# Optimization experiments

Measured on AMD Instinct MI355X. Metric: run time of the kernel, lower is better.

## Reference

```python
import jax, jax.numpy as jnp
import numpy as np

N_NODES = 100000
N_EDGES = 640000
D_IN = 128
D_OUT = 128


def setup_inputs() -> dict:
    key = jax.random.key(0)
    k1, k2, k3, k4, k5 = jax.random.split(key, 5)
    feats = jax.random.normal(k1, (N_NODES, D_IN), dtype=jnp.float32)
    src = jax.random.randint(k2, (N_EDGES,), 0, N_NODES, dtype=jnp.int32)
    dst = jax.random.randint(k3, (N_EDGES,), 0, N_NODES, dtype=jnp.int32)
    # Xavier-normal-ish init (gain for relu = sqrt(2))
    std = float(np.sqrt(2.0) * np.sqrt(2.0 / (D_IN + D_OUT)))
    linear_skip_weight = jax.random.normal(k4, (D_OUT, D_IN), dtype=jnp.float32) * std
    linear_msg_weight = jax.random.normal(k5, (D_OUT, D_IN), dtype=jnp.float32) * std
    linear_skip_bias = jnp.zeros((D_OUT,), dtype=jnp.float32)
    linear_msg_bias = jnp.zeros((D_OUT,), dtype=jnp.float32)
    return {
        "feats": feats,
        "src": src,
        "dst": dst,
        "linear_skip_weight": linear_skip_weight,
        "linear_skip_bias": linear_skip_bias,
        "linear_msg_weight": linear_msg_weight,
        "linear_msg_bias": linear_msg_bias,
    }


def reference(feats, src, dst, linear_skip_weight, linear_skip_bias,
              linear_msg_weight, linear_msg_bias):
    n = feats.shape[0]
    # degree from scatter-add of edge weights (ones) at source rows
    deg = jax.ops.segment_sum(jnp.ones_like(src, dtype=feats.dtype), src,
                              num_segments=n)
    deg_inv_sqrt = jnp.where(deg > 0, jax.lax.rsqrt(jnp.maximum(deg, 1.0)) * (deg > 0), 0.0)
    deg_inv_sqrt = jnp.where(deg > 0, deg ** -0.5, 0.0)
    # normalize source features, gather along edges, scatter-sum to dst
    feat_src = feats * deg_inv_sqrt[:, None]           # [N, D_IN]
    msgs = feat_src[src]                               # [E, D_IN]
    rst = jax.ops.segment_sum(msgs, dst, num_segments=n)  # [N, D_IN]
    rst = rst * deg_inv_sqrt[:, None]
    rst_ = rst @ linear_msg_weight.T + linear_msg_bias
    skip_x = feats @ linear_skip_weight.T + linear_skip_bias
    return rst_ + skip_x
```

## Files before the change

kernel.cpp:

```cpp
#include <hip/hip_runtime.h>

#define N_NODES 100000
#define N_EDGES 640000
#define D 128
#define NB ((N_NODES + 1023) / 1024)
#define BKT_C 16
#define OVF_CAP 32768

typedef short v8s __attribute__((ext_vector_type(8)));
typedef float v4f __attribute__((ext_vector_type(4)));

__device__ __forceinline__ unsigned short f2bf(float x) {
    unsigned int u = __builtin_bit_cast(unsigned int, x);
    u += 0x7fffu + ((u >> 16) & 1u);
    return (unsigned short)(u >> 16);
}
__device__ __forceinline__ float bf2f(unsigned int hi) {
    return __builtin_bit_cast(float, hi << 16);
}

__global__ __launch_bounds__(256) void k_zero(int4* __restrict__ pk4,
                                              int* __restrict__ ovf_cnt) {
    int i = blockIdx.x * blockDim.x + threadIdx.x;
    if (i < N_NODES / 4) pk4[i] = make_int4(0, 0, 0, 0);
    if (i == 0) *ovf_cnt = 0;
}

__global__ __launch_bounds__(256) void k_pre(const float* __restrict__ feats,
                                             const float* __restrict__ Wm,
                                             const float* __restrict__ Ws,
                                             const float* __restrict__ bmsg,
                                             const float* __restrict__ bskip,
                                             const int* __restrict__ src,
                                             const int* __restrict__ dst,
                                             unsigned int* __restrict__ pk,
                                             unsigned short* __restrict__ Bcat,
                                             float* __restrict__ bias,
                                             char* __restrict__ outb,
                                             int* __restrict__ bucket,
                                             int* __restrict__ ovf_cnt,
                                             int2* __restrict__ ovf) {
    int i = blockIdx.x * blockDim.x + threadIdx.x;
    if (i < D * D) {
        int j = i >> 7;
        int k = i & 127;
        Bcat[j * 256 + k]       = f2bf(Wm[i]);
        Bcat[j * 256 + 128 + k] = f2bf(Ws[i]);
    }
    if (i < D) bias[i] = bmsg[i] + bskip[i];
    if (i < N_EDGES) {
        int s = src[i];
        int d = dst[i];
        atomicAdd(&pk[s], 1u);
        unsigned int old = atomicAdd(&pk[d], 0x10000u);
        if (bucket) {
            unsigned int p = old >> 16;
            if (p < BKT_C) {
                bucket[d * BKT_C + (int)p] = s;
            } else {
                int q = atomicAdd(ovf_cnt, 1);
                if (q < OVF_CAP) ovf[q] = make_int2(d, s);
            }
        }
    }
    int g = i * 8;
    int row = g >> 7;
    int col = g & 127;
    if (row < N_NODES) {
        const float4* sp = (const float4*)(feats + g);
        float4 x = sp[0], y = sp[1];
        uint4 p;
        p.x = (unsigned)f2bf(x.x) | ((unsigned)f2bf(x.y) << 16);
        p.y = (unsigned)f2bf(x.z) | ((unsigned)f2bf(x.w) << 16);
        p.z = (unsigned)f2bf(y.x) | ((unsigned)f2bf(y.y) << 16);
        p.w = (unsigned)f2bf(y.z) | ((unsigned)f2bf(y.w) << 16);
        *(uint4*)(outb + (size_t)row * 512 + 256 + col * 2) = p;
    }
}

__global__ __launch_bounds__(256) void k_scan1(const unsigned int* __restrict__ pk,
                                               int* __restrict__ rowptr,
                                               int* __restrict__ bsums) {
    __shared__ int sd[256];
    int t = threadIdx.x;
    int i0 = blockIdx.x * 1024 + t * 4;
    int v[4];
    int s = 0;
#pragma unroll
    for (int q = 0; q < 4; q++) {
        int i = i0 + q;
        v[q] = (i < N_NODES) ? (int)(pk[i] >> 16) : 0;
        s += v[q];
    }
    sd[t] = s;
    __syncthreads();
    for (int off = 1; off < 256; off <<= 1) {
        int y = (t >= off) ? sd[t - off] : 0;
        __syncthreads();
        sd[t] += y;
        __syncthreads();
    }
    int run = sd[t] - s;
    if (t == 255) bsums[blockIdx.x] = sd[255];
#pragma unroll
    for (int q = 0; q < 4; q++) {
        int i = i0 + q;
        if (i < N_NODES) rowptr[i] = run;
        run += v[q];
    }
}

__global__ __launch_bounds__(128) void k_scan2(int* __restrict__ bsums) {
    __shared__ int sd[128];
    int t = threadIdx.x;
    int v = (t < NB) ? bsums[t] : 0;
    sd[t] = v;
    __syncthreads();
    for (int off = 1; off < 128; off <<= 1) {
        int y = (t >= off) ? sd[t - off] : 0;
        __syncthreads();
        sd[t] += y;
        __syncthreads();
    }
    if (t < NB) bsums[t] = sd[t] - v;
}

__global__ __launch_bounds__(256) void k_scan3(const int* __restrict__ bsums,
                                               int* __restrict__ rowptr) {
    int add = bsums[blockIdx.x];
    int i0 = blockIdx.x * 1024 + threadIdx.x * 4;
#pragma unroll
    for (int q = 0; q < 4; q++) {
        int i = i0 + q;
        if (i < N_NODES) rowptr[i] += add;
    }
}

__global__ __launch_bounds__(256) void k_fill(const int* __restrict__ src,
                                              const int* __restrict__ dst,
                                              int* __restrict__ rowptr,
                                              int* __restrict__ csr_src) {
    int e = blockIdx.x * blockDim.x + threadIdx.x;
    if (e < N_EDGES) {
        int p = atomicAdd(&rowptr[dst[e]], 1);
        csr_src[p] = src[e];
    }
}

__device__ __forceinline__ void agg_edge(const char* outb,
                                         const unsigned int* pk,
                                         int s, int sub, float* acc) {
    float sc = rsqrtf((float)(pk[s] & 0xffffu));
    uint4 v = *(const uint4*)(outb + (size_t)s * 512 + 256 + sub * 16);
    acc[0] += bf2f(v.x & 0xffffu) * sc;
    acc[1] += bf2f(v.x >> 16) * sc;
    acc[2] += bf2f(v.y & 0xffffu) * sc;
    acc[3] += bf2f(v.y >> 16) * sc;
    acc[4] += bf2f(v.z & 0xffffu) * sc;
    acc[5] += bf2f(v.z >> 16) * sc;
    acc[6] += bf2f(v.w & 0xffffu) * sc;
    acc[7] += bf2f(v.w >> 16) * sc;
}

__device__ __forceinline__ void agg_finish(char* outb, int wid,
                                           unsigned int pkn, int grp, int sub,
                                           float* acc) {
#pragma unroll
    for (int i = 0; i < 8; i++) {
        acc[i] += __shfl_xor(acc[i], 16);
        acc[i] += __shfl_xor(acc[i], 32);
    }
    if (grp == 0) {
        int dsrc = (int)(pkn & 0xffffu);
        float scn = (dsrc > 0) ? rsqrtf((float)dsrc) : 0.0f;
        uint4 p;
        p.x = (unsigned)f2bf(acc[0] * scn) | ((unsigned)f2bf(acc[1] * scn) << 16);
        p.y = (unsigned)f2bf(acc[2] * scn) | ((unsigned)f2bf(acc[3] * scn) << 16);
        p.z = (unsigned)f2bf(acc[4] * scn) | ((unsigned)f2bf(acc[5] * scn) << 16);
        p.w = (unsigned)f2bf(acc[6] * scn) | ((unsigned)f2bf(acc[7] * scn) << 16);
        *(uint4*)(outb + (size_t)wid * 512 + sub * 16) = p;
    }
}

__global__ __launch_bounds__(256) void k_agg_bkt(char* __restrict__ outb,
                                                 const unsigned int* __restrict__ pk,
                                                 const int* __restrict__ bucket,
                                                 const int* __restrict__ ovf_cnt,
                                                 const int2* __restrict__ ovf) {
    int wid = (int)((blockIdx.x * (unsigned)blockDim.x + threadIdx.x) >> 6);
    int lane = threadIdx.x & 63;
    if (wid >= N_NODES) return;
    int grp = lane >> 4;
    int sub = lane & 15;
    unsigned int pkn = pk[wid];
    int cnt = (int)(pkn >> 16);
    int m = cnt < BKT_C ? cnt : BKT_C;
    const int* bk = bucket + wid * BKT_C;
    float acc[8];
#pragma unroll
    for (int i = 0; i < 8; i++) acc[i] = 0.f;

    for (int base = 0; base < m; base += 4) {
        int e = base + grp;
        if (e < m) agg_edge(outb, pk, bk[e], sub, acc);
    }
    if (cnt > BKT_C) {
        int no = *ovf_cnt;
        if (no > OVF_CAP) no = OVF_CAP;
        for (int i = grp; i < no; i += 4) {
            int2 p = ovf[i];
            if (p.x == wid) agg_edge(outb, pk, p.y, sub, acc);
        }
    }
    agg_finish(outb, wid, pkn, grp, sub, acc);
}

__global__ __launch_bounds__(256) void k_agg_csr(char* __restrict__ outb,
                                                 const unsigned int* __restrict__ pk,
                                                 const int* __restrict__ rowptr,
                                                 const int* __restrict__ csr_src) {
    int wid = (int)((blockIdx.x * (unsigned)blockDim.x + threadIdx.x) >> 6);
    int lane = threadIdx.x & 63;
    if (wid >= N_NODES) return;
    int grp = lane >> 4;
    int sub = lane & 15;
    int start = (wid == 0) ? 0 : rowptr[wid - 1];
    int end = rowptr[wid];
    float acc[8];
#pragma unroll
    for (int i = 0; i < 8; i++) acc[i] = 0.f;
    for (int base = start; base < end; base += 4) {
        int e = base + grp;
        if (e < end) agg_edge(outb, pk, csr_src[e], sub, acc);
    }
    agg_finish(outb, wid, pk[wid], grp, sub, acc);
}

__global__ __launch_bounds__(256) void k_gemm(const unsigned short* __restrict__ Bcat,
                                              const float* __restrict__ bias,
                                              float* __restrict__ outf) {
    __shared__ unsigned short Bl[128][264];
    const char* Ab = (const char*)outf;
    int tid = threadIdx.x;
    int lane = tid & 63;
    int w = tid >> 6;
    int n0 = blockIdx.x * 128;

    for (int i = tid; i < 128 * 32; i += 256) {
        int r = i >> 5, c = i & 31;
        *(uint4*)(&Bl[r][c * 8]) = *(const uint4*)(Bcat + r * 256 + c * 8);
    }
    __syncthreads();

    int q = lane >> 4;
    int lr = lane & 15;

    int r0 = n0 + w * 32 + lr;      if (r0 > N_NODES - 1) r0 = N_NODES - 1;
    int r1 = n0 + w * 32 + 16 + lr; if (r1 > N_NODES - 1) r1 = N_NODES - 1;
    const char* a0p = Ab + (size_t)r0 * 512 + q * 16;
    const char* a1p = Ab + (size_t)r1 * 512 + q * 16;

    v4f acc[2][8];
#pragma unroll
    for (int mt = 0; mt < 2; mt++)
#pragma unroll
        for (int t = 0; t < 8; t++) acc[mt][t] = (v4f){0.f, 0.f, 0.f, 0.f};

#pragma unroll
    for (int kk = 0; kk < 8; kk++) {
        v8s a0 = *(const v8s*)(a0p + kk * 64);
        v8s a1 = *(const v8s*)(a1p + kk * 64);
#pragma unroll
        for (int t = 0; t < 8; t++) {
            v8s b = *(const v8s*)(&Bl[t * 16 + lr][kk * 32 + q * 8]);
            acc[0][t] = __builtin_amdgcn_mfma_f32_16x16x32_bf16(a0, b, acc[0][t], 0, 0, 0);
            acc[1][t] = __builtin_amdgcn_mfma_f32_16x16x32_bf16(a1, b, acc[1][t], 0, 0, 0);
        }
    }

#pragma unroll
    for (int t = 0; t < 8; t++) {
        float bv = bias[t * 16 + lr];
#pragma unroll
        for (int mt = 0; mt < 2; mt++) {
            int rowb = n0 + w * 32 + mt * 16 + q * 4;
#pragma unroll
            for (int r = 0; r < 4; r++) {
                int row = rowb + r;
                if (row < N_NODES)
                    outf[(size_t)row * 128 + t * 16 + lr] = acc[mt][t][r] + bv;
            }
        }
    }
}

extern "C" void kernel_launch(void* const* d_in, const int* in_sizes, int n_in,
                              void* d_out, int out_size, void* d_ws, size_t ws_size,
                              hipStream_t stream) {
    const float* feats = (const float*)d_in[0];
    const int*   src   = (const int*)d_in[1];
    const int*   dst   = (const int*)d_in[2];
    const float* Wskip = (const float*)d_in[3];
    const float* bskip = (const float*)d_in[4];
    const float* Wmsg  = (const float*)d_in[5];
    const float* bmsg  = (const float*)d_in[6];

    char* w = (char*)d_ws;

    bool pathA = ws_size >= (size_t)7128320;

    if (pathA) {
        unsigned int*   pk      = (unsigned int*)w;
        int*            ovf_cnt = (int*)(w + 400000);
        unsigned short* Bcat    = (unsigned short*)(w + 400128);
        float*          bias    = (float*)(w + 465664);
        int*            bucket  = (int*)(w + 466176);
        int2*           ovf     = (int2*)(w + 6866176);

        hipLaunchKernelGGL(k_zero, dim3((N_NODES / 4 + 255) / 256), dim3(256), 0,
                           stream, (int4*)pk, ovf_cnt);
        hipLaunchKernelGGL(k_pre, dim3((N_NODES * (D / 8) + 255) / 256), dim3(256),
                           0, stream, feats, Wmsg, Wskip, bmsg, bskip, src, dst, pk,
                           Bcat, bias, (char*)d_out, bucket, ovf_cnt, ovf);
        hipLaunchKernelGGL(k_agg_bkt, dim3((N_NODES * 64 + 255) / 256), dim3(256), 0,
                           stream, (char*)d_out, pk, bucket, ovf_cnt, ovf);
        hipLaunchKernelGGL(k_gemm, dim3((N_NODES + 127) / 128), dim3(256), 0, stream,
                           Bcat, bias, (float*)d_out);
    } else {
        unsigned int*   pk      = (unsigned int*)w;
        int*            rowptr  = (int*)(w + 400000);
        int*            bsums   = (int*)(w + 800128);
        unsigned short* Bcat    = (unsigned short*)(w + 800640);
        float*          bias    = (float*)(w + 866176);
        int*            csr_src = (int*)(w + 866688);

        hipLaunchKernelGGL(k_zero, dim3((N_NODES / 4 + 255) / 256), dim3(256), 0,
                           stream, (int4*)pk, (int*)(w + 400000) );
        hipLaunchKernelGGL(k_pre, dim3((N_NODES * (D / 8) + 255) / 256), dim3(256),
                           0, stream, feats, Wmsg, Wskip, bmsg, bskip, src, dst, pk,
                           Bcat, bias, (char*)d_out, (int*)nullptr, (int*)nullptr,
                           (int2*)nullptr);
        hipLaunchKernelGGL(k_scan1, dim3(NB), dim3(256), 0, stream, pk, rowptr,
                           bsums);
        hipLaunchKernelGGL(k_scan2, dim3(1), dim3(128), 0, stream, bsums);
        hipLaunchKernelGGL(k_scan3, dim3(NB), dim3(256), 0, stream, bsums, rowptr);
        hipLaunchKernelGGL(k_fill, dim3((N_EDGES + 255) / 256), dim3(256), 0, stream,
                           src, dst, rowptr, csr_src);
        hipLaunchKernelGGL(k_agg_csr, dim3((N_NODES * 64 + 255) / 256), dim3(256), 0,
                           stream, (char*)d_out, pk, rowptr, csr_src);
        hipLaunchKernelGGL(k_gemm, dim3((N_NODES + 127) / 128), dim3(256), 0, stream,
                           Bcat, bias, (float*)d_out);
    }
}
```

Baseline: 236.1 us.

## Compute source degrees via LDS histogram kernels instead of global atomics

Source-degree counting moves out of k_pre's global atomics into a new k_hist kernel. It builds per-range LDS histograms over edge slices, and k_comb sums the partial counts and precomputes deg^-1/2 into a float array. The aggregation kernel then reads this precomputed scale instead of unpacking the degree and calling rsqrt per edge. This halves the global atomics in the pre-pass but adds two kernel launches and a pass over src, and the overflow capacity is reduced.

```diff
diff --git a/kernel.cpp b/kernel.cpp
--- a/kernel.cpp
+++ b/kernel.cpp
@@ -5,7 +5,11 @@
 #define D 128
 #define NB ((N_NODES + 1023) / 1024)
 #define BKT_C 16
-#define OVF_CAP 32768
+#define OVF_CAP 16384
+#define NRG 16
+#define NRN (N_NODES / NRG)
+#define NSL 8
+#define ESL (N_EDGES / NSL)
 
 typedef short v8s __attribute__((ext_vector_type(8)));
 typedef float v4f __attribute__((ext_vector_type(4)));
@@ -24,6 +28,38 @@
     int i = blockIdx.x * blockDim.x + threadIdx.x;
     if (i < N_NODES / 4) pk4[i] = make_int4(0, 0, 0, 0);
     if (i == 0) *ovf_cnt = 0;
+}
+
+__global__ __launch_bounds__(1024) void k_hist(const int* __restrict__ src,
+                                               unsigned int* __restrict__ partials) {
+    __shared__ unsigned int h[NRN];
+    int tid = threadIdx.x;
+    int r = blockIdx.x / NSL;
+    int sl = blockIdx.x % NSL;
+    for (int i = tid; i < NRN; i += 1024) h[i] = 0;
+    __syncthreads();
+    int n0 = r * NRN;
+    int e0 = sl * ESL;
+    for (int i = tid; i < ESL; i += 1024) {
+        unsigned int rel = (unsigned int)(src[e0 + i] - n0);
+        if (rel < NRN) atomicAdd(&h[rel], 1u);
+    }
+    __syncthreads();
+    unsigned int* dp = partials + (size_t)blockIdx.x * NRN;
+    for (int i = tid; i < NRN; i += 1024) dp[i] = h[i];
+}
+
+__global__ __launch_bounds__(256) void k_comb(const unsigned int* __restrict__ partials,
+                                              float* __restrict__ dis) {
+    int n = blockIdx.x * blockDim.x + threadIdx.x;
+    if (n >= N_NODES) return;
+    int r = n / NRN;
+    int rel = n - r * NRN;
+    unsigned int a = 0;
+#pragma unroll
+    for (int sl = 0; sl < NSL; sl++)
+        a += partials[(size_t)(r * NSL + sl) * NRN + rel];
+    dis[n] = (a > 0) ? rsqrtf((float)a) : 0.0f;
 }
 
 __global__ __launch_bounds__(256) void k_pre(const float* __restrict__ feats,
@@ -51,16 +87,17 @@
     if (i < N_EDGES) {
         int s = src[i];
         int d = dst[i];
-        atomicAdd(&pk[s], 1u);
-        unsigned int old = atomicAdd(&pk[d], 0x10000u);
         if (bucket) {
-            unsigned int p = old >> 16;
+            unsigned int p = atomicAdd(&pk[d], 1u);
             if (p < BKT_C) {
                 bucket[d * BKT_C + (int)p] = s;
             } else {
                 int q = atomicAdd(ovf_cnt, 1);
                 if (q < OVF_CAP) ovf[q] = make_int2(d, s);
             }
+        } else {
+            atomicAdd(&pk[s], 1u);
+            atomicAdd(&pk[d], 0x10000u);
         }
     }
     int g = i * 8;
@@ -147,9 +184,24 @@
     }
 }
 
-__device__ __forceinline__ void agg_edge(const char* outb,
-                                         const unsigned int* pk,
-                                         int s, int sub, float* acc) {
+__device__ __forceinline__ void agg_edge_dis(const char* outb,
+                                             const float* dis,
+                                             int s, int sub, float* acc) {
+    float sc = dis[s];
+    uint4 v = *(const uint4*)(outb + (size_t)s * 512 + 256 + sub * 16);
+    acc[0] += bf2f(v.x & 0xffffu) * sc;
+    acc[1] += bf2f(v.x >> 16) * sc;
+    acc[2] += bf2f(v.y & 0xffffu) * sc;
+    acc[3] += bf2f(v.y >> 16) * sc;
+    acc[4] += bf2f(v.z & 0xffffu) * sc;
+    acc[5] += bf2f(v.z >> 16) * sc;
+    acc[6] += bf2f(v.w & 0xffffu) * sc;
+    acc[7] += bf2f(v.w >> 16) * sc;
+}
+
+__device__ __forceinline__ void agg_edge_pk(const char* outb,
+                                            const unsigned int* pk,
+                                            int s, int sub, float* acc) {
     float sc = rsqrtf((float)(pk[s] & 0xffffu));
     uint4 v = *(const uint4*)(outb + (size_t)s * 512 + 256 + sub * 16);
     acc[0] += bf2f(v.x & 0xffffu) * sc;
@@ -162,17 +214,14 @@
     acc[7] += bf2f(v.w >> 16) * sc;
 }
 
-__device__ __forceinline__ void agg_finish(char* outb, int wid,
-                                           unsigned int pkn, int grp, int sub,
-                                           float* acc) {
+__device__ __forceinline__ void agg_finish(char* outb, int wid, float scn,
+                                           int grp, int sub, float* acc) {
 #pragma unroll
     for (int i = 0; i < 8; i++) {
         acc[i] += __shfl_xor(acc[i], 16);
         acc[i] += __shfl_xor(acc[i], 32);
     }
     if (grp == 0) {
-        int dsrc = (int)(pkn & 0xffffu);
-        float scn = (dsrc > 0) ? rsqrtf((float)dsrc) : 0.0f;
         uint4 p;
         p.x = (unsigned)f2bf(acc[0] * scn) | ((unsigned)f2bf(acc[1] * scn) << 16);
         p.y = (unsigned)f2bf(acc[2] * scn) | ((unsigned)f2bf(acc[3] * scn) << 16);
@@ -184,6 +233,7 @@
 
 __global__ __launch_bounds__(256) void k_agg_bkt(char* __restrict__ outb,
                                                  const unsigned int* __restrict__ pk,
+                                                 const float* __restrict__ dis,
                                                  const int* __restrict__ bucket,
                                                  const int* __restrict__ ovf_cnt,
                                                  const int2* __restrict__ ovf) {
@@ -192,8 +242,7 @@
     if (wid >= N_NODES) return;
     int grp = lane >> 4;
     int sub = lane & 15;
-    unsigned int pkn = pk[wid];
-    int cnt = (int)(pkn >> 16);
+    int cnt = (int)pk[wid];
     int m = cnt < BKT_C ? cnt : BKT_C;
     const int* bk = bucket + wid * BKT_C;
     float acc[8];
@@ -202,17 +251,17 @@
 
     for (int base = 0; base < m; base += 4) {
         int e = base + grp;
-        if (e < m) agg_edge(outb, pk, bk[e], sub, acc);
+        if (e < m) agg_edge_dis(outb, dis, bk[e], sub, acc);
     }
     if (cnt > BKT_C) {
         int no = *ovf_cnt;
         if (no > OVF_CAP) no = OVF_CAP;
         for (int i = grp; i < no; i += 4) {
             int2 p = ovf[i];
-            if (p.x == wid) agg_edge(outb, pk, p.y, sub, acc);
+            if (p.x == wid) agg_edge_dis(outb, dis, p.y, sub, acc);
         }
     }
-    agg_finish(outb, wid, pkn, grp, sub, acc);
+    agg_finish(outb, wid, dis[wid], grp, sub, acc);
 }
 
 __global__ __launch_bounds__(256) void k_agg_csr(char* __restrict__ outb,
@@ -231,9 +280,11 @@
     for (int i = 0; i < 8; i++) acc[i] = 0.f;
     for (int base = start; base < end; base += 4) {
         int e = base + grp;
-        if (e < end) agg_edge(outb, pk, csr_src[e], sub, acc);
-    }
-    agg_finish(outb, wid, pk[wid], grp, sub, acc);
+        if (e < end) agg_edge_pk(outb, pk, csr_src[e], sub, acc);
+    }
+    int dsrc = (int)(pk[wid] & 0xffffu);
+    float scn = (dsrc > 0) ? rsqrtf((float)dsrc) : 0.0f;
+    agg_finish(outb, wid, scn, grp, sub, acc);
 }
 
 __global__ __launch_bounds__(256) void k_gemm(const unsigned short* __restrict__ Bcat,
@@ -307,23 +358,29 @@
 
     char* w = (char*)d_ws;
 
-    bool pathA = ws_size >= (size_t)7128320;
+    bool pathA = ws_size >= (size_t)7397248;
 
     if (pathA) {
-        unsigned int*   pk      = (unsigned int*)w;
-        int*            ovf_cnt = (int*)(w + 400000);
-        unsigned short* Bcat    = (unsigned short*)(w + 400128);
-        float*          bias    = (float*)(w + 465664);
-        int*            bucket  = (int*)(w + 466176);
-        int2*           ovf     = (int2*)(w + 6866176);
+        unsigned int*   pk       = (unsigned int*)w;
+        float*          dis      = (float*)(w + 400000);
+        int*            ovf_cnt  = (int*)(w + 800000);
+        unsigned short* Bcat     = (unsigned short*)(w + 800128);
+        float*          bias     = (float*)(w + 865664);
+        int*            bucket   = (int*)(w + 866176);
+        unsigned int*   partials = (unsigned int*)(w + 866176);
+        int2*           ovf      = (int2*)(w + 7266176);
 
         hipLaunchKernelGGL(k_zero, dim3((N_NODES / 4 + 255) / 256), dim3(256), 0,
                            stream, (int4*)pk, ovf_cnt);
+        hipLaunchKernelGGL(k_hist, dim3(NRG * NSL), dim3(1024), 0, stream, src,
+                           partials);
+        hipLaunchKernelGGL(k_comb, dim3((N_NODES + 255) / 256), dim3(256), 0, stream,
+                           partials, dis);
         hipLaunchKernelGGL(k_pre, dim3((N_NODES * (D / 8) + 255) / 256), dim3(256),
                            0, stream, feats, Wmsg, Wskip, bmsg, bskip, src, dst, pk,
                            Bcat, bias, (char*)d_out, bucket, ovf_cnt, ovf);
         hipLaunchKernelGGL(k_agg_bkt, dim3((N_NODES * 64 + 255) / 256), dim3(256), 0,
-                           stream, (char*)d_out, pk, bucket, ovf_cnt, ovf);
+                           stream, (char*)d_out, pk, dis, bucket, ovf_cnt, ovf);
         hipLaunchKernelGGL(k_gemm, dim3((N_NODES + 127) / 128), dim3(256), 0, stream,
                            Bcat, bias, (float*)d_out);
     } else {
@@ -335,7 +392,7 @@
         int*            csr_src = (int*)(w + 866688);
 
         hipLaunchKernelGGL(k_zero, dim3((N_NODES / 4 + 255) / 256), dim3(256), 0,
-                           stream, (int4*)pk, (int*)(w + 400000) );
+                           stream, (int4*)pk, (int*)(w + 400000));
         hipLaunchKernelGGL(k_pre, dim3((N_NODES * (D / 8) + 255) / 256), dim3(256),
                            0, stream, feats, Wmsg, Wskip, bmsg, bskip, src, dst, pk,
                            Bcat, bias, (char*)d_out, (int*)nullptr, (int*)nullptr,
```

New measurement: 243.2 us. 3.0% more time.
